# Kernel optimization log

Measured on AMD Instinct MI355X. Metric: run time of the kernel, lower is better.

## Reference

```python
import jax, jax.numpy as jnp
import numpy as np

H_DIM = 1024
N_HEADS = 16
SEQ_LEN = 2048
BATCH = 4


def setup_inputs() -> dict:
    key = jax.random.key(0)
    ks = jax.random.split(key, 9)
    s = 1.0 / np.sqrt(H_DIM)
    return {
        "x": jax.random.normal(ks[0], (BATCH, SEQ_LEN, H_DIM), dtype=jnp.float32),
        "Wq": jax.random.normal(ks[1], (H_DIM, H_DIM), dtype=jnp.float32) * s,
        "bq": jax.random.normal(ks[2], (H_DIM,), dtype=jnp.float32) * 0.01,
        "Wk": jax.random.normal(ks[3], (H_DIM, H_DIM), dtype=jnp.float32) * s,
        "bk": jax.random.normal(ks[4], (H_DIM,), dtype=jnp.float32) * 0.01,
        "Wv": jax.random.normal(ks[5], (H_DIM, H_DIM), dtype=jnp.float32) * s,
        "bv": jax.random.normal(ks[6], (H_DIM,), dtype=jnp.float32) * 0.01,
        "Wo": jax.random.normal(ks[7], (H_DIM, H_DIM), dtype=jnp.float32) * s,
        "bo": jax.random.normal(ks[8], (H_DIM,), dtype=jnp.float32) * 0.01,
    }


def reference(x, Wq, bq, Wk, bk, Wv, bv, Wo, bo):
    B, T, C = x.shape
    N = N_HEADS
    D = C // N
    # projections -> [B, N, T, D]
    def split_heads(t):
        return t.reshape(B, T, N, D).transpose(0, 2, 1, 3)
    q = split_heads(x @ Wq + bq)
    k = split_heads(x @ Wk + bk)
    v = split_heads(x @ Wv + bv)
    scale = 1.0 / jnp.sqrt(jnp.asarray(D, dtype=x.dtype))
    logits = jnp.einsum("bntd,bnsd->bnts", q, k) * scale  # [B,N,T,T]
    causal = jnp.tril(jnp.ones((T, T), dtype=bool))
    logits = jnp.where(causal[None, None], logits, jnp.asarray(-jnp.inf, dtype=x.dtype))
    attn = jax.nn.softmax(logits, axis=-1)
    ctx = jnp.einsum("bnts,bnsd->bntd", attn, v)  # [B,N,T,D]
    ctx = ctx.transpose(0, 2, 1, 3).reshape(B, T, C)
    return ctx @ Wo + bo
```

## Files before the change

kernel.cpp:

```cpp
#include <hip/hip_runtime.h>
#include <hip/hip_bf16.h>


typedef __attribute__((ext_vector_type(8))) short bhalf8;
typedef __attribute__((ext_vector_type(4))) float f32x4;

#define BATCH 4
#define SEQ 2048
#define CDIM 1024
#define NHEAD 16
#define HDIM 64
#define MTOT (BATCH * SEQ)
#define QSCALE 0.18033688011112042f

static __device__ inline unsigned short f2bf(float f) {
    unsigned int u = __float_as_uint(f);
    unsigned int r = (u + 0x7fffu + ((u >> 16) & 1u)) >> 16;
    return (unsigned short)r;
}
static __device__ inline float bf2f(unsigned short u) {
    return __uint_as_float(((unsigned int)u) << 16);
}
static __device__ inline f32x4 zero4() {
    f32x4 z = {0.f, 0.f, 0.f, 0.f};
    return z;
}
static __device__ inline f32x4 MFMA(bhalf8 a, bhalf8 b, f32x4 c) {
    return __builtin_amdgcn_mfma_f32_16x16x32_bf16(a, b, c, 0, 0, 0);
}
static __device__ inline void gload16(const void* g, void* l) {
    __builtin_amdgcn_global_load_lds(
        (const __attribute__((address_space(1))) unsigned int*)g,
        (__attribute__((address_space(3))) unsigned int*)l, 16, 0, 0);
}
static __device__ inline unsigned int pkbf16(float lo, float hi) {
    union { __hip_bfloat162 h; unsigned int u; } c;
    c.h = __float22bfloat162_rn(make_float2(lo, hi));
    return c.u;
}

__global__ __launch_bounds__(256) void cast_x_kernel(const float* __restrict__ x,
                                                     short* __restrict__ o, int n8) {
    int i = blockIdx.x * 256 + threadIdx.x;
    if (i >= n8) return;
    const float4* xv = (const float4*)x;
    float4 a = xv[i * 2];
    float4 b = xv[i * 2 + 1];
    bhalf8 r;
    r[0] = (short)f2bf(a.x); r[1] = (short)f2bf(a.y);
    r[2] = (short)f2bf(a.z); r[3] = (short)f2bf(a.w);
    r[4] = (short)f2bf(b.x); r[5] = (short)f2bf(b.y);
    r[6] = (short)f2bf(b.z); r[7] = (short)f2bf(b.w);
    *(bhalf8*)(o + (size_t)i * 8) = r;
}

__global__ __launch_bounds__(256) void wtrans_kernel(const float* __restrict__ W0,
                                                     const float* __restrict__ W1,
                                                     const float* __restrict__ W2,
                                                     const float* __restrict__ W3,
                                                     short* __restrict__ out) {
    __shared__ float t[32][33];
    const float* W = (blockIdx.z == 0) ? W0 : (blockIdx.z == 1) ? W1
                     : (blockIdx.z == 2) ? W2 : W3;
    short* o = out + (size_t)blockIdx.z * CDIM * CDIM;
    int n0 = blockIdx.x * 32, k0 = blockIdx.y * 32;
    int tx = threadIdx.x, ty = threadIdx.y;
    for (int j = 0; j < 4; ++j)
        t[ty + j * 8][tx] = W[(size_t)(k0 + ty + j * 8) * CDIM + n0 + tx];
    __syncthreads();
    for (int j = 0; j < 4; ++j)
        o[(size_t)(n0 + ty + j * 8) * CDIM + k0 + tx] = (short)f2bf(t[tx][ty + j * 8]);
}

template <int MODE, int GN>
__global__ __launch_bounds__(512) void gemm256(const short* __restrict__ A,
                                               const short* __restrict__ Bt,
                                               const float* __restrict__ b0,
                                               const float* __restrict__ b1,
                                               const float* __restrict__ b2,
                                               unsigned short* __restrict__ QKout,
                                               unsigned short* __restrict__ Vout,
                                               float* __restrict__ Fout) {
    __shared__ char lds[65536];
    char* AlB0 = lds;
    char* BlB0 = lds + 32768;

    const int tid = threadIdx.x, lane = tid & 63, w = tid >> 6;
    const int g = lane >> 4, t16 = lane & 15;
    const int wr = w >> 2, wc = w & 3;

    const int f = blockIdx.x;
    const int xcd = f & 7, i = f >> 3;
    const int mt = xcd * 4 + i / GN, nt = i % GN;
    const int tm = mt * 256, tn = nt * 256;
    const int part = nt >> 2;

    const int c0 = tid, c1 = 512 + tid;
    const int r0 = c0 >> 2, r1 = c1 >> 2;
    const int k0c = (c0 & 3) ^ ((r0 >> 1) & 3);
    const int k1c = (c1 & 3) ^ ((r1 >> 1) & 3);
    const short* a0 = A + (size_t)(tm + r0) * 1024 + k0c * 8;
    const short* a1 = A + (size_t)(tm + r1) * 1024 + k1c * 8;
    const short* bp0 = Bt + (size_t)(tn + r0) * 1024 + k0c * 8;
    const short* bp1 = Bt + (size_t)(tn + r1) * 1024 + k1c * 8;

    int aoff[8], boff[4];
#pragma unroll
    for (int mi = 0; mi < 8; ++mi) {
        int row = wr * 128 + mi * 16 + t16;
        aoff[mi] = row * 64 + ((g ^ ((row >> 1) & 3)) << 4);
    }
#pragma unroll
    for (int ni = 0; ni < 4; ++ni) {
        int row = wc * 64 + ni * 16 + t16;
        boff[ni] = row * 64 + ((g ^ ((row >> 1) & 3)) << 4);
    }

    f32x4 acc[8][4];
#pragma unroll
    for (int mi = 0; mi < 8; ++mi)
#pragma unroll
        for (int ni = 0; ni < 4; ++ni) acc[mi][ni] = zero4();

#define STAGE(kt_, bb_)                                                   \
    do {                                                                  \
        int off_ = (kt_) * 32;                                            \
        char* al_ = AlB0 + (bb_) * 16384;                                 \
        char* bl_ = BlB0 + (bb_) * 16384;                                 \
        gload16(a0 + off_, al_ + w * 1024);                               \
        gload16(a1 + off_, al_ + 8192 + w * 1024);                        \
        gload16(bp0 + off_, bl_ + w * 1024);                              \
        gload16(bp1 + off_, bl_ + 8192 + w * 1024);                       \
    } while (0)

    STAGE(0, 0);
    __syncthreads();

#pragma unroll 2
    for (int kt = 0; kt < 32; ++kt) {
        const int buf = kt & 1;
        if (kt + 1 < 32) STAGE(kt + 1, buf ^ 1);
        const char* al = AlB0 + buf * 16384;
        const char* bl = BlB0 + buf * 16384;
        bhalf8 af[8], bfr[4];
#pragma unroll
        for (int mi = 0; mi < 8; ++mi) af[mi] = *(const bhalf8*)(al + aoff[mi]);
#pragma unroll
        for (int ni = 0; ni < 4; ++ni) bfr[ni] = *(const bhalf8*)(bl + boff[ni]);
        __builtin_amdgcn_s_setprio(1);
#pragma unroll
        for (int mi = 0; mi < 8; ++mi)
#pragma unroll
            for (int ni = 0; ni < 4; ++ni)
                acc[mi][ni] = MFMA(af[mi], bfr[ni], acc[mi][ni]);
        __builtin_amdgcn_s_setprio(0);
        __syncthreads();
    }
#undef STAGE

    for (int h = 0; h < 2; ++h) {
        if (h) __syncthreads();
        if (MODE == 0 && part == 2) {
            if (wr == h) {
#pragma unroll
                for (int mi = 0; mi < 8; ++mi)
#pragma unroll
                    for (int ni = 0; ni < 4; ++ni) {
                        int col = wc * 64 + ni * 16 + t16;
                        float bias = b2[(tn + col) & 1023];
#pragma unroll
                        for (int r = 0; r < 4; ++r) {
                            int m_l = mi * 16 + g * 4 + r;
                            int byte = col * 256 + ((m_l * 2) ^ ((col & 7) << 4));
                            *(unsigned short*)(lds + byte) = f2bf(acc[mi][ni][r] + bias);
                        }
                    }
            }
            __syncthreads();
#pragma unroll
            for (int p = 0; p < 8; ++p) {
                int lin = p * 8192 + tid * 16;
                int rv = lin >> 8;
                int inrow = lin & 255;
                int phys = rv * 256 + (inrow ^ ((rv & 7) << 4));
                bhalf8 val = *(const bhalf8*)(lds + phys);
                int m0 = inrow >> 1;
                int n_g = tn + rv;
                int hh = (n_g & 1023) >> 6, d = n_g & 63;
                int m = tm + h * 128 + m0;
                int bi = m >> 11, t0 = m & 2047;
                *(bhalf8*)(Vout + (((size_t)((bi * NHEAD + hh) * HDIM + d)) << 11) + t0) = val;
            }
        } else {
            if (wr == h) {
#pragma unroll
                for (int mi = 0; mi < 8; ++mi)
#pragma unroll
                    for (int ni = 0; ni < 4; ++ni) {
                        int col = wc * 64 + ni * 16 + t16;
                        float bias = 0.f;
                        if (MODE == 0) bias = (part == 0 ? b0 : b1)[(tn + col) & 1023];
#pragma unroll
                        for (int r = 0; r < 4; ++r) {
                            int row_l = mi * 16 + g * 4 + r;
                            float v = acc[mi][ni][r] + bias;
                            if (MODE == 0 && part == 0) v *= QSCALE;
                            int byte = row_l * 512 + ((col * 2) ^ (((row_l >> 2) & 3) << 5));
                            *(unsigned short*)(lds + byte) = f2bf(v);
                        }
                    }
            }
            __syncthreads();
#pragma unroll
            for (int p = 0; p < 8; ++p) {
                int lin = p * 8192 + tid * 16;
                int row_l = lin >> 9;
                int inrow = lin & 511;
                int phys = row_l * 512 + ((inrow & ~31) ^ (((row_l >> 2) & 3) << 5)) + (inrow & 31);
                bhalf8 val = *(const bhalf8*)(lds + phys);
                int col0 = inrow >> 1;
                int n_g = tn + col0;
                int m = tm + h * 128 + row_l;
                if (MODE == 1) {
                    float* op = Fout + (size_t)m * 1024 + n_g;
                    float4 o0, o1;
                    o0.x = bf2f((unsigned short)val[0]) + b0[n_g + 0];
                    o0.y = bf2f((unsigned short)val[1]) + b0[n_g + 1];
                    o0.z = bf2f((unsigned short)val[2]) + b0[n_g + 2];
                    o0.w = bf2f((unsigned short)val[3]) + b0[n_g + 3];
                    o1.x = bf2f((unsigned short)val[4]) + b0[n_g + 4];
                    o1.y = bf2f((unsigned short)val[5]) + b0[n_g + 5];
                    o1.z = bf2f((unsigned short)val[6]) + b0[n_g + 6];
                    o1.w = bf2f((unsigned short)val[7]) + b0[n_g + 7];
                    *(float4*)(op) = o0;
                    *(float4*)(op + 4) = o1;
                } else {
                    int bi = m >> 11, t = m & 2047;
                    int hh = (n_g & 1023) >> 6, d0 = n_g & 63;
                    *(bhalf8*)(QKout +
                               (((size_t)((part * 64 + bi * NHEAD + hh) * SEQ + t)) << 6) + d0) = val;
                }
            }
        }
    }
}

__global__ __launch_bounds__(256) void attn_kernel(const short* __restrict__ Q,
                                                   const short* __restrict__ K,
                                                   const short* __restrict__ V,
                                                   unsigned short* __restrict__ ctx) {
    __shared__ short Kl[2][64 * 64];
    __shared__ short Vl[2][64 * 64];
    __shared__ short Pl[4][16 * 64];

    const int tid = threadIdx.x, lane = tid & 63, w = tid >> 6;
    const int g = lane >> 4, t16 = lane & 15;

    int orig = blockIdx.x;
    int swz = (orig & 7) * 128 + (orig >> 3);
    const int bh = swz >> 4;
    const int sp = swz & 15;

    const short* Qh = Q + ((size_t)bh << 17);
    const short* Kh = K + ((size_t)bh << 17);
    const short* Vh = V + ((size_t)bh << 17);

    int koff[2], voff[2], ldst[2];
#pragma unroll
    for (int it = 0; it < 2; ++it) {
        int c = it * 256 + tid;
        int srow = c >> 3;
        int dc = (c & 7) ^ (srow & 7);
        koff[it] = (srow << 6) + dc * 8;
        voff[it] = (srow << 11) + dc * 8;
        ldst[it] = it * 4096 + w * 1024;
    }

#define STAGE(kv_, bb_)                                                       \
    do {                                                                      \
        gload16(Kh + koff[0] + ((kv_) << 12), (char*)Kl[bb_] + ldst[0]);      \
        gload16(Kh + koff[1] + ((kv_) << 12), (char*)Kl[bb_] + ldst[1]);      \
        gload16(Vh + voff[0] + ((kv_) << 6), (char*)Vl[bb_] + ldst[0]);       \
        gload16(Vh + voff[1] + ((kv_) << 6), (char*)Vl[bb_] + ldst[1]);       \
    } while (0)

    const int b = bh >> 4, hh = bh & 15;
    const int swb = (t16 & 7) << 4;

    int buf = 0;
    STAGE(0, 0);

    for (int ph = 0; ph < 2; ++ph) {
        const int qti = (ph == 0) ? (31 - sp) : sp;
        const int qbase = qti * 64;
        const int ntile = qti + 1;

        bhalf8 qf0, qf1;
        {
            const short* qp = Qh + ((size_t)(qbase + w * 16 + t16) << 6) + g * 8;
            qf0 = *(const bhalf8*)(qp);
            qf1 = *(const bhalf8*)(qp + 32);
        }

        f32x4 acc[4];
#pragma unroll
        for (int i = 0; i < 4; ++i) acc[i] = zero4();
        float l = 0.f;

        __syncthreads();

        for (int kv = 0; kv < ntile; ++kv) {
            if (kv + 1 < ntile) STAGE(kv + 1, buf ^ 1);

            f32x4 lg[4];
            __builtin_amdgcn_s_setprio(1);
#pragma unroll
            for (int cb = 0; cb < 4; ++cb) {
                int s = cb * 16 + t16;
                int sw = (s & 7) << 4;
                const char* rowp = (const char*)Kl[buf] + s * 128;
                bhalf8 k0 = *(const bhalf8*)(rowp + ((g * 16) ^ sw));
                bhalf8 k1 = *(const bhalf8*)(rowp + ((64 + g * 16) ^ sw));
                f32x4 z = zero4();
                z = MFMA(k0, qf0, z);
                z = MFMA(k1, qf1, z);
                lg[cb] = z;
            }
            __builtin_amdgcn_s_setprio(0);

            if (kv == qti) {
                int rowl = w * 16 + t16;
#pragma unroll
                for (int cb = 0; cb < 4; ++cb) {
                    int key0 = cb * 16 + g * 4;
#pragma unroll
                    for (int r = 0; r < 4; ++r)
                        if (key0 + r > rowl) lg[cb][r] = -1e30f;
                }
            }

            {
                float s_ = 0.f;
                int rowbyte = t16 * 128;
#pragma unroll
                for (int cb = 0; cb < 4; ++cb) {
                    float e0 = exp2f(lg[cb][0]);
                    float e1 = exp2f(lg[cb][1]);
                    float e2 = exp2f(lg[cb][2]);
                    float e3 = exp2f(lg[cb][3]);
                    s_ += (e0 + e1) + (e2 + e3);
                    uint2 wv;
                    wv.x = pkbf16(e0, e1);
                    wv.y = pkbf16(e2, e3);
                    int byte = (rowbyte + cb * 32 + g * 8) ^ swb;
                    *(uint2*)((char*)Pl[w] + byte) = wv;
                }
                l += s_;
            }

            __builtin_amdgcn_s_setprio(1);
#pragma unroll
            for (int kk = 0; kk < 2; ++kk) {
                bhalf8 vf[4];
#pragma unroll
                for (int db = 0; db < 4; ++db) {
                    int d = db * 16 + t16;
                    int vbyte = d * 128 + ((kk * 64 + g * 16) ^ ((d & 7) << 4));
                    vf[db] = *(const bhalf8*)((const char*)Vl[buf] + vbyte);
                }
                int abyte = (t16 * 128 + kk * 64 + g * 16) ^ swb;
                bhalf8 pa = *(const bhalf8*)((const char*)Pl[w] + abyte);
#pragma unroll
                for (int db = 0; db < 4; ++db)
                    acc[db] = MFMA(pa, vf[db], acc[db]);
            }
            __builtin_amdgcn_s_setprio(0);

            __syncthreads();
            buf ^= 1;
        }

        if (ph == 0) STAGE(0, buf);

        float lt = l;
        lt += __shfl_xor(lt, 16, 64);
        lt += __shfl_xor(lt, 32, 64);
        float linv = 1.f / lt;
#pragma unroll
        for (int r = 0; r < 4; ++r) {
            float inv = __shfl(linv, g * 4 + r, 64);
            int t = qbase + w * 16 + g * 4 + r;
            size_t rowoff = (((size_t)(b * SEQ + t)) << 10) + hh * 64;
#pragma unroll
            for (int db = 0; db < 4; ++db)
                ctx[rowoff + db * 16 + t16] = f2bf(acc[db][r] * inv);
        }
    }
#undef STAGE
}

extern "C" void kernel_launch(void* const* d_in, const int* in_sizes, int n_in,
                              void* d_out, int out_size, void* d_ws, size_t ws_size,
                              hipStream_t stream) {
    const float* x  = (const float*)d_in[0];
    const float* Wq = (const float*)d_in[1];
    const float* bq = (const float*)d_in[2];
    const float* Wk = (const float*)d_in[3];
    const float* bk = (const float*)d_in[4];
    const float* Wv = (const float*)d_in[5];
    const float* bv = (const float*)d_in[6];
    const float* Wo = (const float*)d_in[7];
    const float* bo = (const float*)d_in[8];

    char* ws = (char*)d_ws;
    short* x16 = (short*)(ws);
    short* Wt  = (short*)(ws + (size_t)16 * 1024 * 1024);
    short* Wot = Wt + (size_t)3 * CDIM * CDIM;
    short* Qb  = (short*)(ws + (size_t)24 * 1024 * 1024);
    short* Vb  = (short*)(ws + (size_t)56 * 1024 * 1024);
    short* Ctx = (short*)(ws + (size_t)72 * 1024 * 1024);

    cast_x_kernel<<<dim3(MTOT * CDIM / 8 / 256), dim3(256), 0, stream>>>(
        x, x16, MTOT * CDIM / 8);
    wtrans_kernel<<<dim3(32, 32, 4), dim3(32, 8), 0, stream>>>(Wq, Wk, Wv, Wo, Wt);

    gemm256<0, 12><<<dim3(384), dim3(512), 0, stream>>>(
        x16, Wt, bq, bk, bv, (unsigned short*)Qb, (unsigned short*)Vb, nullptr);

    attn_kernel<<<dim3(1024), dim3(256), 0, stream>>>(
        Qb, Qb + (size_t)64 * SEQ * HDIM, Vb, (unsigned short*)Ctx);

    gemm256<1, 4><<<dim3(128), dim3(512), 0, stream>>>(
        Ctx, Wot, bo, nullptr, nullptr, nullptr, nullptr, (float*)d_out);
}
```

Measured before the change: 215.1 us.

## Shrink projection GEMM tiles from 256x256 to 128x128 with 256-thread blocks

Replaces the 256x256-tile, 512-thread GEMM with a 128x128-tile, 256-thread variant, and adjusts the grid mapping, LDS staging and epilogue to match. The output projection rises from 128 to 512 blocks and the QKV projection from 384 to 1536, so the MI355X's 256 CUs get fuller coverage and less tail imbalance. In exchange, each block reuses A and B less per load, adding L2/global traffic and giving a lower MFMA-to-load ratio.

```diff
diff --git a/kernel.cpp b/kernel.cpp
--- a/kernel.cpp
+++ b/kernel.cpp
@@ -73,7 +73,7 @@
 }
 
 template <int MODE, int GN>
-__global__ __launch_bounds__(512) void gemm256(const short* __restrict__ A,
+__global__ __launch_bounds__(256) void gemm128(const short* __restrict__ A,
                                                const short* __restrict__ Bt,
                                                const float* __restrict__ b0,
                                                const float* __restrict__ b1,
@@ -81,21 +81,22 @@
                                                unsigned short* __restrict__ QKout,
                                                unsigned short* __restrict__ Vout,
                                                float* __restrict__ Fout) {
-    __shared__ char lds[65536];
+    __shared__ char lds[32768];
     char* AlB0 = lds;
-    char* BlB0 = lds + 32768;
+    char* BlB0 = lds + 16384;
 
     const int tid = threadIdx.x, lane = tid & 63, w = tid >> 6;
     const int g = lane >> 4, t16 = lane & 15;
-    const int wr = w >> 2, wc = w & 3;
+    const int wr = w >> 1, wc = w & 1;
 
     const int f = blockIdx.x;
     const int xcd = f & 7, i = f >> 3;
-    const int mt = xcd * 4 + i / GN, nt = i % GN;
-    const int tm = mt * 256, tn = nt * 256;
-    const int part = nt >> 2;
-
-    const int c0 = tid, c1 = 512 + tid;
+    const int mt = xcd * 8 + i / GN, nt = i % GN;
+    const int tm = mt * 128, tn = nt * 128;
+    const int part = tn >> 10;
+    const int tnp = tn & 1023;
+
+    const int c0 = tid, c1 = 256 + tid;
     const int r0 = c0 >> 2, r1 = c1 >> 2;
     const int k0c = (c0 & 3) ^ ((r0 >> 1) & 3);
     const int k1c = (c1 & 3) ^ ((r1 >> 1) & 3);
@@ -104,10 +105,10 @@
     const short* bp0 = Bt + (size_t)(tn + r0) * 1024 + k0c * 8;
     const short* bp1 = Bt + (size_t)(tn + r1) * 1024 + k1c * 8;
 
-    int aoff[8], boff[4];
-#pragma unroll
-    for (int mi = 0; mi < 8; ++mi) {
-        int row = wr * 128 + mi * 16 + t16;
+    int aoff[4], boff[4];
+#pragma unroll
+    for (int mi = 0; mi < 4; ++mi) {
+        int row = wr * 64 + mi * 16 + t16;
         aoff[mi] = row * 64 + ((g ^ ((row >> 1) & 3)) << 4);
     }
 #pragma unroll
@@ -116,21 +117,21 @@
         boff[ni] = row * 64 + ((g ^ ((row >> 1) & 3)) << 4);
     }
 
-    f32x4 acc[8][4];
-#pragma unroll
-    for (int mi = 0; mi < 8; ++mi)
+    f32x4 acc[4][4];
+#pragma unroll
+    for (int mi = 0; mi < 4; ++mi)
 #pragma unroll
         for (int ni = 0; ni < 4; ++ni) acc[mi][ni] = zero4();
 
 #define STAGE(kt_, bb_)                                                   \
     do {                                                                  \
         int off_ = (kt_) * 32;                                            \
-        char* al_ = AlB0 + (bb_) * 16384;                                 \
-        char* bl_ = BlB0 + (bb_) * 16384;                                 \
-        gload16(a0 + off_, al_ + w * 1024);                               \
-        gload16(a1 + off_, al_ + 8192 + w * 1024);                        \
-        gload16(bp0 + off_, bl_ + w * 1024);                              \
-        gload16(bp1 + off_, bl_ + 8192 + w * 1024);                       \
+        char* al_ = AlB0 + (bb_) * 8192;                                  \
+        char* bl_ = BlB0 + (bb_) * 8192;                                  \
+        gload16(a0 + off_, al_ + tid * 16);                               \
+        gload16(a1 + off_, al_ + 4096 + tid * 16);                        \
+        gload16(bp0 + off_, bl_ + tid * 16);                              \
+        gload16(bp1 + off_, bl_ + 4096 + tid * 16);                       \
     } while (0)
 
     STAGE(0, 0);
@@ -140,16 +141,16 @@
     for (int kt = 0; kt < 32; ++kt) {
         const int buf = kt & 1;
         if (kt + 1 < 32) STAGE(kt + 1, buf ^ 1);
-        const char* al = AlB0 + buf * 16384;
-        const char* bl = BlB0 + buf * 16384;
-        bhalf8 af[8], bfr[4];
-#pragma unroll
-        for (int mi = 0; mi < 8; ++mi) af[mi] = *(const bhalf8*)(al + aoff[mi]);
+        const char* al = AlB0 + buf * 8192;
+        const char* bl = BlB0 + buf * 8192;
+        bhalf8 af[4], bfr[4];
+#pragma unroll
+        for (int mi = 0; mi < 4; ++mi) af[mi] = *(const bhalf8*)(al + aoff[mi]);
 #pragma unroll
         for (int ni = 0; ni < 4; ++ni) bfr[ni] = *(const bhalf8*)(bl + boff[ni]);
         __builtin_amdgcn_s_setprio(1);
 #pragma unroll
-        for (int mi = 0; mi < 8; ++mi)
+        for (int mi = 0; mi < 4; ++mi)
 #pragma unroll
             for (int ni = 0; ni < 4; ++ni)
                 acc[mi][ni] = MFMA(af[mi], bfr[ni], acc[mi][ni]);
@@ -158,88 +159,81 @@
     }
 #undef STAGE
 
-    for (int h = 0; h < 2; ++h) {
-        if (h) __syncthreads();
-        if (MODE == 0 && part == 2) {
-            if (wr == h) {
-#pragma unroll
-                for (int mi = 0; mi < 8; ++mi)
-#pragma unroll
-                    for (int ni = 0; ni < 4; ++ni) {
-                        int col = wc * 64 + ni * 16 + t16;
-                        float bias = b2[(tn + col) & 1023];
-#pragma unroll
-                        for (int r = 0; r < 4; ++r) {
-                            int m_l = mi * 16 + g * 4 + r;
-                            int byte = col * 256 + ((m_l * 2) ^ ((col & 7) << 4));
-                            *(unsigned short*)(lds + byte) = f2bf(acc[mi][ni][r] + bias);
-                        }
-                    }
-            }
-            __syncthreads();
-#pragma unroll
-            for (int p = 0; p < 8; ++p) {
-                int lin = p * 8192 + tid * 16;
-                int rv = lin >> 8;
-                int inrow = lin & 255;
-                int phys = rv * 256 + (inrow ^ ((rv & 7) << 4));
-                bhalf8 val = *(const bhalf8*)(lds + phys);
-                int m0 = inrow >> 1;
-                int n_g = tn + rv;
-                int hh = (n_g & 1023) >> 6, d = n_g & 63;
-                int m = tm + h * 128 + m0;
-                int bi = m >> 11, t0 = m & 2047;
-                *(bhalf8*)(Vout + (((size_t)((bi * NHEAD + hh) * HDIM + d)) << 11) + t0) = val;
-            }
-        } else {
-            if (wr == h) {
-#pragma unroll
-                for (int mi = 0; mi < 8; ++mi)
-#pragma unroll
-                    for (int ni = 0; ni < 4; ++ni) {
-                        int col = wc * 64 + ni * 16 + t16;
-                        float bias = 0.f;
-                        if (MODE == 0) bias = (part == 0 ? b0 : b1)[(tn + col) & 1023];
-#pragma unroll
-                        for (int r = 0; r < 4; ++r) {
-                            int row_l = mi * 16 + g * 4 + r;
-                            float v = acc[mi][ni][r] + bias;
-                            if (MODE == 0 && part == 0) v *= QSCALE;
-                            int byte = row_l * 512 + ((col * 2) ^ (((row_l >> 2) & 3) << 5));
-                            *(unsigned short*)(lds + byte) = f2bf(v);
-                        }
-                    }
-            }
-            __syncthreads();
-#pragma unroll
-            for (int p = 0; p < 8; ++p) {
-                int lin = p * 8192 + tid * 16;
-                int row_l = lin >> 9;
-                int inrow = lin & 511;
-                int phys = row_l * 512 + ((inrow & ~31) ^ (((row_l >> 2) & 3) << 5)) + (inrow & 31);
-                bhalf8 val = *(const bhalf8*)(lds + phys);
-                int col0 = inrow >> 1;
+    if (MODE == 0 && part == 2) {
+#pragma unroll
+        for (int mi = 0; mi < 4; ++mi)
+#pragma unroll
+            for (int ni = 0; ni < 4; ++ni) {
+                int col_l = wc * 64 + ni * 16 + t16;
+                float bias = b2[tnp + col_l];
+#pragma unroll
+                for (int r = 0; r < 4; ++r) {
+                    int row_l = wr * 64 + mi * 16 + g * 4 + r;
+                    int byte = col_l * 256 + ((row_l * 2) ^ ((col_l & 7) << 4));
+                    *(unsigned short*)(lds + byte) = f2bf(acc[mi][ni][r] + bias);
+                }
+            }
+        __syncthreads();
+#pragma unroll
+        for (int p = 0; p < 8; ++p) {
+            int lin = p * 4096 + tid * 16;
+            int rv = lin >> 8;
+            int inrow = lin & 255;
+            int phys = rv * 256 + (inrow ^ ((rv & 7) << 4));
+            bhalf8 val = *(const bhalf8*)(lds + phys);
+            int n_g = tnp + rv;
+            int hh = n_g >> 6, d = n_g & 63;
+            int m = tm + (inrow >> 1);
+            int bi = m >> 11, t0 = m & 2047;
+            *(bhalf8*)(Vout + (((size_t)((bi * NHEAD + hh) * HDIM + d)) << 11) + t0) = val;
+        }
+    } else {
+#pragma unroll
+        for (int mi = 0; mi < 4; ++mi)
+#pragma unroll
+            for (int ni = 0; ni < 4; ++ni) {
+                int col_l = wc * 64 + ni * 16 + t16;
+                float bias = 0.f;
+                if (MODE == 0) bias = (part == 0 ? b0 : b1)[tnp + col_l];
+#pragma unroll
+                for (int r = 0; r < 4; ++r) {
+                    int row_l = wr * 64 + mi * 16 + g * 4 + r;
+                    float v = acc[mi][ni][r] + bias;
+                    if (MODE == 0 && part == 0) v *= QSCALE;
+                    int byte = row_l * 256 + ((col_l * 2) ^ (((row_l >> 2) & 3) << 5));
+                    *(unsigned short*)(lds + byte) = f2bf(v);
+                }
+            }
+        __syncthreads();
+#pragma unroll
+        for (int p = 0; p < 8; ++p) {
+            int lin = p * 4096 + tid * 16;
+            int row_l = lin >> 8;
+            int inrow = lin & 255;
+            int phys = row_l * 256 + ((inrow & ~31) ^ (((row_l >> 2) & 3) << 5)) + (inrow & 31);
+            bhalf8 val = *(const bhalf8*)(lds + phys);
+            int col0 = inrow >> 1;
+            int m = tm + row_l;
+            if (MODE == 1) {
                 int n_g = tn + col0;
-                int m = tm + h * 128 + row_l;
-                if (MODE == 1) {
-                    float* op = Fout + (size_t)m * 1024 + n_g;
-                    float4 o0, o1;
-                    o0.x = bf2f((unsigned short)val[0]) + b0[n_g + 0];
-                    o0.y = bf2f((unsigned short)val[1]) + b0[n_g + 1];
-                    o0.z = bf2f((unsigned short)val[2]) + b0[n_g + 2];
-                    o0.w = bf2f((unsigned short)val[3]) + b0[n_g + 3];
-                    o1.x = bf2f((unsigned short)val[4]) + b0[n_g + 4];
-                    o1.y = bf2f((unsigned short)val[5]) + b0[n_g + 5];
-                    o1.z = bf2f((unsigned short)val[6]) + b0[n_g + 6];
-                    o1.w = bf2f((unsigned short)val[7]) + b0[n_g + 7];
-                    *(float4*)(op) = o0;
-                    *(float4*)(op + 4) = o1;
-                } else {
-                    int bi = m >> 11, t = m & 2047;
-                    int hh = (n_g & 1023) >> 6, d0 = n_g & 63;
-                    *(bhalf8*)(QKout +
-                               (((size_t)((part * 64 + bi * NHEAD + hh) * SEQ + t)) << 6) + d0) = val;
-                }
+                float* op = Fout + (size_t)m * 1024 + n_g;
+                float4 o0, o1;
+                o0.x = bf2f((unsigned short)val[0]) + b0[n_g + 0];
+                o0.y = bf2f((unsigned short)val[1]) + b0[n_g + 1];
+                o0.z = bf2f((unsigned short)val[2]) + b0[n_g + 2];
+                o0.w = bf2f((unsigned short)val[3]) + b0[n_g + 3];
+                o1.x = bf2f((unsigned short)val[4]) + b0[n_g + 4];
+                o1.y = bf2f((unsigned short)val[5]) + b0[n_g + 5];
+                o1.z = bf2f((unsigned short)val[6]) + b0[n_g + 6];
+                o1.w = bf2f((unsigned short)val[7]) + b0[n_g + 7];
+                *(float4*)(op) = o0;
+                *(float4*)(op + 4) = o1;
+            } else {
+                int n_g = tnp + col0;
+                int bi = m >> 11, t = m & 2047;
+                int hh = n_g >> 6, d0 = n_g & 63;
+                *(bhalf8*)(QKout +
+                           (((size_t)((part * 64 + bi * NHEAD + hh) * SEQ + t)) << 6) + d0) = val;
             }
         }
     }
@@ -424,12 +418,12 @@
         x, x16, MTOT * CDIM / 8);
     wtrans_kernel<<<dim3(32, 32, 4), dim3(32, 8), 0, stream>>>(Wq, Wk, Wv, Wo, Wt);
 
-    gemm256<0, 12><<<dim3(384), dim3(512), 0, stream>>>(
+    gemm128<0, 24><<<dim3(1536), dim3(256), 0, stream>>>(
         x16, Wt, bq, bk, bv, (unsigned short*)Qb, (unsigned short*)Vb, nullptr);
 
     attn_kernel<<<dim3(1024), dim3(256), 0, stream>>>(
         Qb, Qb + (size_t)64 * SEQ * HDIM, Vb, (unsigned short*)Ctx);
 
-    gemm256<1, 4><<<dim3(128), dim3(512), 0, stream>>>(
+    gemm128<1, 8><<<dim3(512), dim3(256), 0, stream>>>(
         Ctx, Wot, bo, nullptr, nullptr, nullptr, nullptr, (float*)d_out);
 }
```

Result: faster. 191.9 us (-10.8%).
